# Optimization experiments

Measured on AMD Instinct MI355X. Metric: run time of the kernel, lower is better.

Reference implementation:

```python
import jax, jax.numpy as jnp
import numpy as np

DIM = 2048
N_HEADS = 16
Q_LORA = 1536
KV_LORA = 512
NOPE = 128
ROPE = 64
QK_HD = NOPE + ROPE  # 192
V_HD = 128
BS, SEQ = 2, 2048
EPS = 1e-6


def rmsnorm(x, w):
    var = jnp.mean(jnp.square(x), axis=-1, keepdims=True)
    return x * jax.lax.rsqrt(var + EPS) * w


def rope_cos_sin(seq_len, dim, dtype):
    inv_freq = 1.0 / (10000.0 ** (jnp.arange(0, dim, 2, dtype=jnp.float32) / dim))
    t = jnp.arange(seq_len, dtype=jnp.float32)
    freqs = jnp.outer(t, inv_freq)            # [S, dim/2]
    emb = jnp.concatenate([freqs, freqs], -1)  # [S, dim]
    return jnp.cos(emb).astype(dtype), jnp.sin(emb).astype(dtype)


def rotate_half(x):
    x1, x2 = jnp.split(x, 2, axis=-1)
    return jnp.concatenate([-x2, x1], axis=-1)


def apply_rope(x, cos, sin):
    # x: [B, S, H, D]; cos/sin: [S, D] -> broadcast over B, H
    return x * cos[None, :, None, :] + rotate_half(x) * sin[None, :, None, :]


def setup_inputs() -> dict:
    key = jax.random.key(0)
    ks = jax.random.split(key, 8)
    s = 0.02
    return {
        "x": jax.random.normal(ks[0], (BS, SEQ, DIM), jnp.float32),
        "wq_a_w": jax.random.normal(ks[1], (Q_LORA, DIM), jnp.float32) * s,
        "wq_a_b": jnp.zeros((Q_LORA,), jnp.float32),
        "q_norm_w": jnp.ones((Q_LORA,), jnp.float32),
        "wq_b_w": jax.random.normal(ks[2], (N_HEADS * QK_HD, Q_LORA), jnp.float32) * s,
        "wq_b_b": jnp.zeros((N_HEADS * QK_HD,), jnp.float32),
        "wkv_a_w": jax.random.normal(ks[3], (KV_LORA + ROPE, DIM), jnp.float32) * s,
        "wkv_a_b": jnp.zeros((KV_LORA + ROPE,), jnp.float32),
        "kv_norm_w": jnp.ones((KV_LORA,), jnp.float32),
        "wkv_b_w": jax.random.normal(ks[4], (N_HEADS * (NOPE + V_HD), KV_LORA), jnp.float32) * s,
        "wkv_b_b": jnp.zeros((N_HEADS * (NOPE + V_HD),), jnp.float32),
        "wo_w": jax.random.normal(ks[5], (DIM, N_HEADS * V_HD), jnp.float32) * s,
        "wo_b": jnp.zeros((DIM,), jnp.float32),
    }


def reference(x, wq_a_w, wq_a_b, q_norm_w, wq_b_w, wq_b_b,
              wkv_a_w, wkv_a_b, kv_norm_w, wkv_b_w, wkv_b_b, wo_w, wo_b):
    bs, seq_len, _ = x.shape
    # Q path: low-rank down, RMSNorm, up
    q = x @ wq_a_w.T + wq_a_b
    q = rmsnorm(q, q_norm_w)
    q = q @ wq_b_w.T + wq_b_b
    q = q.reshape(bs, seq_len, N_HEADS, QK_HD)
    q_nope, q_pe = q[..., :NOPE], q[..., NOPE:]
    # KV path: joint low-rank + decoupled rope key
    kv = x @ wkv_a_w.T + wkv_a_b
    kv_c, k_pe = kv[..., :KV_LORA], kv[..., KV_LORA:]
    k_pe = k_pe[:, :, None, :]  # [B, S, 1, ROPE]
    cos, sin = rope_cos_sin(seq_len, ROPE, x.dtype)
    q_pe = apply_rope(q_pe, cos, sin)
    k_pe = apply_rope(k_pe, cos, sin)
    # naive mode: materialize per-head K/V
    kv_c = rmsnorm(kv_c, kv_norm_w)
    kvb = (kv_c @ wkv_b_w.T + wkv_b_b).reshape(bs, seq_len, N_HEADS, NOPE + V_HD)
    k_nope, v = kvb[..., :NOPE], kvb[..., NOPE:]
    q_full = jnp.concatenate([q_nope, q_pe], axis=-1)            # [B,S,H,192]
    k_full = jnp.concatenate(
        [k_nope, jnp.broadcast_to(k_pe, (bs, seq_len, N_HEADS, ROPE))], axis=-1)
    scale = 1.0 / np.sqrt(QK_HD)
    scores = jnp.einsum('bqhd,bkhd->bhqk', q_full, k_full) * scale
    causal = jnp.tril(jnp.ones((seq_len, seq_len), bool))
    scores = jnp.where(causal[None, None], scores, jnp.finfo(scores.dtype).min)
    attn = jax.nn.softmax(scores, axis=-1)
    out = jnp.einsum('bhqk,bkhd->bqhd', attn, v)
    out = out.reshape(bs, seq_len, N_HEADS * V_HD)
    return out @ wo_w.T + wo_b
```

## Files before the change

kernel.cpp:

```cpp
#include <hip/hip_runtime.h>

#define SEQ 2048
#define NHEADS 16

typedef __bf16 bf16;
typedef __bf16 bf16x8 __attribute__((ext_vector_type(8)));
typedef __bf16 bf16x4v __attribute__((ext_vector_type(4)));
typedef float f32x4 __attribute__((ext_vector_type(4)));
typedef unsigned short u16x4 __attribute__((ext_vector_type(4)));

static __device__ __forceinline__ float bf2f(unsigned short u) {
    union { unsigned u32; float f; } v; v.u32 = ((unsigned)u) << 16; return v.f;
}
static __device__ __forceinline__ unsigned short f2bf(float f) {
    union { float f; unsigned u; } v; v.f = f;
    unsigned u = v.u;
    unsigned r = u + 0x7fffu + ((u >> 16) & 1u);
    return (unsigned short)(r >> 16);
}

static __device__ __forceinline__ void g2l16(const unsigned short* g, unsigned short* l) {
    __builtin_amdgcn_global_load_lds(
        (const __attribute__((address_space(1))) unsigned int*)(unsigned long long)g,
        (__attribute__((address_space(3))) unsigned int*)(unsigned int)(unsigned long long)l,
        16, 0, 0);
}

__global__ void detect_dtype(const unsigned* __restrict__ qnw, int* __restrict__ flag) {
    if (threadIdx.x == 0 && blockIdx.x == 0)
        *flag = (qnw[0] == 0x3F800000u) ? 1 : 0;
}

struct CvtArgs {
    const void* src[13];
    unsigned short* dst[13];
    int n[13];
    int startblk[14];
};
__global__ __launch_bounds__(256) void to_bf16_all(CvtArgs a, const int* __restrict__ flag) {
    int bx = blockIdx.x;
    int t = 0;
    while (bx >= a.startblk[t + 1]) ++t;
    int base = (bx - a.startblk[t]) * 4096;
    int n = a.n[t];
    int hi = base + 4096; if (hi > n) hi = n;
    int cnt = hi - base;
    if (*flag) {
        const f32x4* s = (const f32x4*)a.src[t] + (base >> 2);
        u16x4* d = (u16x4*)(a.dst[t] + base);
        int c4 = cnt >> 2;
        for (int e = threadIdx.x; e < c4; e += 256) {
            f32x4 v = s[e];
            u16x4 o;
#pragma unroll
            for (int j = 0; j < 4; ++j) o[j] = f2bf(v[j]);
            d[e] = o;
        }
    } else {
        const uint4* s = (const uint4*)a.src[t] + (base >> 3);
        uint4* d = (uint4*)(a.dst[t] + base);
        int c8 = cnt >> 3;
        for (int e = threadIdx.x; e < c8; e += 256) d[e] = s[e];
    }
}

struct GemmP {
    const unsigned short* A; int lda;
    const unsigned short* W;
    const unsigned short* bias;
    unsigned short* C; float* Cf; int ldc;
    int N; int K; const int* flagp;
    int nbx;
};

static __device__ void gemm_body(const GemmP g, int bx, int by,
                                 unsigned short* Al, unsigned short* Bl)
{
    const int lane = threadIdx.x & 63;
    const int w    = threadIdx.x >> 6;
    const int r    = lane & 15;
    const int quad = lane >> 4;
    const int m0 = by << 7;
    const int n0 = bx << 7;
    const int wr = (w >> 1) << 6;
    const int wc = (w & 1) << 6;

    const int srow = lane >> 2;
    const int scol = (lane & 3) << 3;
    const int j0 = w * 2, j1 = w * 2 + 1;

    const unsigned short* a0 = g.A + (size_t)(m0 + j0 * 16 + srow) * g.lda + scol;
    const unsigned short* a1 = g.A + (size_t)(m0 + j1 * 16 + srow) * g.lda + scol;
    int bn0 = n0 + j0 * 16 + srow; if (bn0 >= g.N) bn0 = g.N - 1;
    int bn1 = n0 + j1 * 16 + srow; if (bn1 >= g.N) bn1 = g.N - 1;
    const unsigned short* b0 = g.W + (size_t)bn0 * g.K + scol;
    const unsigned short* b1 = g.W + (size_t)bn1 * g.K + scol;

    f32x4 acc[4][4];
#pragma unroll
    for (int mt = 0; mt < 4; ++mt)
#pragma unroll
        for (int nt = 0; nt < 4; ++nt) acc[mt][nt] = (f32x4){0.f, 0.f, 0.f, 0.f};

    for (int kb = 0; kb < g.K; kb += 32) {
        __syncthreads();
        g2l16(a0 + kb, &Al[j0 * 512 + lane * 8]);
        g2l16(a1 + kb, &Al[j1 * 512 + lane * 8]);
        g2l16(b0 + kb, &Bl[j0 * 512 + lane * 8]);
        g2l16(b1 + kb, &Bl[j1 * 512 + lane * 8]);
        __syncthreads();

        bf16x8 af[4], bfr[4];
#pragma unroll
        for (int mt = 0; mt < 4; ++mt)
            af[mt] = *(const bf16x8*)&Al[(wr + mt * 16 + r) * 32 + quad * 8];
#pragma unroll
        for (int nt = 0; nt < 4; ++nt)
            bfr[nt] = *(const bf16x8*)&Bl[(wc + nt * 16 + r) * 32 + quad * 8];
#pragma unroll
        for (int mt = 0; mt < 4; ++mt)
#pragma unroll
            for (int nt = 0; nt < 4; ++nt)
                acc[mt][nt] = __builtin_amdgcn_mfma_f32_16x16x32_bf16(af[mt], bfr[nt], acc[mt][nt], 0, 0, 0);
    }

    int outf = (g.Cf && g.flagp) ? *g.flagp : 0;
    float bv[4];
#pragma unroll
    for (int nt = 0; nt < 4; ++nt) {
        int col = n0 + wc + nt * 16 + r;
        bv[nt] = (g.bias && col < g.N) ? bf2f(g.bias[col]) : 0.f;
    }
#pragma unroll
    for (int mt = 0; mt < 4; ++mt) {
#pragma unroll
        for (int i = 0; i < 4; ++i) {
            int row = m0 + wr + mt * 16 + quad * 4 + i;
#pragma unroll
            for (int nt = 0; nt < 4; ++nt) {
                int col = n0 + wc + nt * 16 + r;
                if (col < g.N) {
                    float v = acc[mt][nt][i] + bv[nt];
                    size_t idx = (size_t)row * g.ldc + col;
                    if (g.Cf) {
                        if (outf) g.Cf[idx] = v;
                        else      ((unsigned short*)g.Cf)[idx] = f2bf(v);
                    } else {
                        g.C[idx] = f2bf(v);
                    }
                }
            }
        }
    }
}

__global__ __launch_bounds__(256) void gemm_one(GemmP g) {
    __shared__ unsigned short Al[128 * 32];
    __shared__ unsigned short Bl[128 * 32];
    gemm_body(g, blockIdx.x, blockIdx.y, Al, Bl);
}

__global__ __launch_bounds__(256) void gemm_two(GemmP g0, GemmP g1, int nblk0) {
    __shared__ unsigned short Al[128 * 32];
    __shared__ unsigned short Bl[128 * 32];
    int id = blockIdx.x;
    if (id < nblk0) {
        gemm_body(g0, id % g0.nbx, id / g0.nbx, Al, Bl);
    } else {
        id -= nblk0;
        gemm_body(g1, id % g1.nbx, id / g1.nbx, Al, Bl);
    }
}

__global__ __launch_bounds__(256) void rmsnorm_ip2(
    unsigned short* __restrict__ d0, int s0w, int w0w, const unsigned short* __restrict__ w0,
    unsigned short* __restrict__ d1, int s1w, int w1w, const unsigned short* __restrict__ w1,
    int rows0)
{
    __shared__ float red[256];
    int row = blockIdx.x;
    unsigned short* p; const unsigned short* wt; int stride, width;
    if (row < rows0) { p = d0; wt = w0; stride = s0w; width = w0w; }
    else { row -= rows0; p = d1; wt = w1; stride = s1w; width = w1w; }
    p += (size_t)row * stride;

    float ss = 0.f;
    for (int j = threadIdx.x; j < width; j += 256) {
        float f = bf2f(p[j]);
        ss += f * f;
    }
    red[threadIdx.x] = ss;
    __syncthreads();
    for (int s = 128; s > 0; s >>= 1) {
        if ((int)threadIdx.x < s) red[threadIdx.x] += red[threadIdx.x + s];
        __syncthreads();
    }
    float rstd = rsqrtf(red[0] / (float)width + 1e-6f);
    for (int j = threadIdx.x; j < width; j += 256) {
        p[j] = f2bf(bf2f(p[j]) * rstd * bf2f(wt[j]));
    }
}

__global__ __launch_bounds__(256) void rope_ip_all(
    unsigned short* __restrict__ qbuf, unsigned short* __restrict__ kvbf)
{
    int row = blockIdx.x;
    int s = row & (SEQ - 1);
    for (int t = threadIdx.x; t < 544; t += 256) {
        int i = t & 31;
        float inv = exp2f(-(float)i * (13.2877123795f / 32.0f));
        float ang = (float)s * inv;
        float c = cosf(ang), sn = sinf(ang);
        unsigned short* p;
        if (t < 512) p = qbuf + (size_t)row * 3072 + (t >> 5) * 192 + 128;
        else         p = kvbf + (size_t)row * 576 + 512;
        float x1 = bf2f(p[i]), x2 = bf2f(p[i + 32]);
        p[i]      = f2bf(x1 * c - x2 * sn);
        p[i + 32] = f2bf(x2 * c + x1 * sn);
    }
}

__global__ __launch_bounds__(256) void mla_attn_mfma(
    const unsigned short* __restrict__ qbuf,
    const unsigned short* __restrict__ kvb,
    const unsigned short* __restrict__ kvbuf,
    unsigned short* __restrict__ attn_out)
{
    __shared__ unsigned short Kt[2][32 * 200];
    __shared__ unsigned short Vt[2][128 * 40];
    __shared__ unsigned short Pm[4][16 * 40];

    const int bh = blockIdx.y;
    const int b = bh >> 4, h = bh & 15;
    const int tid  = threadIdx.x;
    const int lane = tid & 63;
    const int w    = tid >> 6;
    const int r    = lane & 15;
    const int quad = lane >> 4;
    const int rowk0 = b * SEQ;
    const float scale = 0.0721687836487f;

    int kldso[3];
    const unsigned short* ksrc[3];
    int krst[3];
#pragma unroll
    for (int j = 0; j < 3; ++j) {
        int v = tid + j * 256;
        int row = v / 24, c = v % 24;
        kldso[j] = row * 200 + c * 8;
        if (c < 16) { ksrc[j] = kvb + (size_t)(rowk0 + row) * 4096 + h * 256 + c * 8; krst[j] = 4096; }
        else        { ksrc[j] = kvbuf + (size_t)(rowk0 + row) * 576 + 512 + (c - 16) * 8; krst[j] = 576; }
    }
    const int vp  = tid & 15;
    const int vdc = tid >> 4;
    const unsigned short* vsrc = kvb + (size_t)(rowk0 + 2 * vp) * 4096 + h * 256 + 128 + vdc * 8;

    unsigned short* Pw = Pm[w];

#pragma unroll 1
    for (int half = 0; half < 2; ++half) {
        const int qt = half ? (31 - (int)blockIdx.x) : (int)blockIdx.x;
        const int qbase = qt * 64 + w * 16;
        const int nkb = 2 * qt + 2;
        const int itmax = 2 * qt + (w >> 1);

        bf16x8 qf[6];
        {
            const unsigned short* qp =
                qbuf + (size_t)(rowk0 + qbase + r) * 3072 + h * 192 + quad * 8;
#pragma unroll
            for (int t = 0; t < 6; ++t) {
                bf16x8 v = *(const bf16x8*)(qp + t * 32);
#pragma unroll
                for (int j = 0; j < 8; ++j) v[j] = (__bf16)((float)v[j] * scale);
                qf[t] = v;
            }
        }

        f32x4 O[8];
#pragma unroll
        for (int f = 0; f < 8; ++f) O[f] = (f32x4){0.f, 0.f, 0.f, 0.f};
        float mi = -1e30f, li = 0.f;

        uint4 pk0, pk1, pk2, pv0, pv1;

        __syncthreads();
        pk0 = *(const uint4*)(ksrc[0]);
        pk1 = *(const uint4*)(ksrc[1]);
        pk2 = *(const uint4*)(ksrc[2]);
        pv0 = *(const uint4*)(vsrc);
        pv1 = *(const uint4*)(vsrc + 4096);
        {
            *(uint4*)&Kt[0][kldso[0]] = pk0;
            *(uint4*)&Kt[0][kldso[1]] = pk1;
            *(uint4*)&Kt[0][kldso[2]] = pk2;
            const unsigned* ea = (const unsigned*)&pv0;
            const unsigned* eb = (const unsigned*)&pv1;
#pragma unroll
            for (int t = 0; t < 4; ++t) {
                unsigned pe = (ea[t] & 0xffffu) | (eb[t] << 16);
                unsigned po = (ea[t] >> 16) | (eb[t] & 0xffff0000u);
                *(unsigned*)&Vt[0][(vdc * 8 + 2 * t) * 40 + 2 * vp]     = pe;
                *(unsigned*)&Vt[0][(vdc * 8 + 2 * t + 1) * 40 + 2 * vp] = po;
            }
        }
        __syncthreads();

#pragma unroll 1
        for (int it = 0; it < nkb; ++it) {
            const int p = it & 1;
            const int kb = it * 32;
            const bool more = (it + 1 < nkb);

            if (more) {
                const size_t koff = (size_t)(kb + 32);
                pk0 = *(const uint4*)(ksrc[0] + koff * krst[0]);
                pk1 = *(const uint4*)(ksrc[1] + koff * krst[1]);
                pk2 = *(const uint4*)(ksrc[2] + koff * krst[2]);
                pv0 = *(const uint4*)(vsrc + koff * 4096);
                pv1 = *(const uint4*)(vsrc + koff * 4096 + 4096);
            }

            if (it <= itmax) {
                f32x4 s0 = {0.f, 0.f, 0.f, 0.f}, s1 = {0.f, 0.f, 0.f, 0.f};
                __builtin_amdgcn_s_setprio(1);
#pragma unroll
                for (int t = 0; t < 6; ++t) {
                    bf16x8 k0 = *(const bf16x8*)&Kt[p][r * 200 + t * 32 + quad * 8];
                    bf16x8 k1 = *(const bf16x8*)&Kt[p][(16 + r) * 200 + t * 32 + quad * 8];
                    s0 = __builtin_amdgcn_mfma_f32_16x16x32_bf16(k0, qf[t], s0, 0, 0, 0);
                    s1 = __builtin_amdgcn_mfma_f32_16x16x32_bf16(k1, qf[t], s1, 0, 0, 0);
                }
                __builtin_amdgcn_s_setprio(0);

                const int qrow = qbase + r;
                float a0[4], a1[4];
                float mx = -1e30f;
                if (kb + 31 > qbase) {
#pragma unroll
                    for (int i = 0; i < 4; ++i) {
                        a0[i] = (kb + quad * 4 + i      <= qrow) ? s0[i] : -1e30f;
                        a1[i] = (kb + 16 + quad * 4 + i <= qrow) ? s1[i] : -1e30f;
                        mx = fmaxf(mx, fmaxf(a0[i], a1[i]));
                    }
                } else {
#pragma unroll
                    for (int i = 0; i < 4; ++i) {
                        a0[i] = s0[i];
                        a1[i] = s1[i];
                        mx = fmaxf(mx, fmaxf(a0[i], a1[i]));
                    }
                }
                mx = fmaxf(mx, __shfl_xor(mx, 16, 64));
                mx = fmaxf(mx, __shfl_xor(mx, 32, 64));

                if (!__all(mx <= mi + 8.f)) {
                    float mn = fmaxf(mi, mx);
                    float al = __expf(mi - mn);
#pragma unroll
                    for (int f = 0; f < 8; ++f) O[f] *= al;
                    li *= al;
                    mi = mn;
                }

                float p0[4], p1[4], ps = 0.f;
#pragma unroll
                for (int i = 0; i < 4; ++i) {
                    p0[i] = __expf(a0[i] - mi);
                    p1[i] = __expf(a1[i] - mi);
                    ps += p0[i] + p1[i];
                }
                ps += __shfl_xor(ps, 16, 64);
                ps += __shfl_xor(ps, 32, 64);
                li += ps;

                bf16x4v b0v, b1v;
#pragma unroll
                for (int i = 0; i < 4; ++i) {
                    b0v[i] = (__bf16)p0[i];
                    b1v[i] = (__bf16)p1[i];
                }
                *(bf16x4v*)&Pw[r * 40 + quad * 4]      = b0v;
                *(bf16x4v*)&Pw[r * 40 + 16 + quad * 4] = b1v;

                bf16x8 pf = *(const bf16x8*)&Pw[r * 40 + quad * 8];
                __builtin_amdgcn_s_setprio(1);
#pragma unroll
                for (int f = 0; f < 8; ++f) {
                    bf16x8 vb = *(const bf16x8*)&Vt[p][(f * 16 + r) * 40 + quad * 8];
                    O[f] = __builtin_amdgcn_mfma_f32_16x16x32_bf16(vb, pf, O[f], 0, 0, 0);
                }
                __builtin_amdgcn_s_setprio(0);
            }

            if (more) {
                const int q2 = 1 - p;
                *(uint4*)&Kt[q2][kldso[0]] = pk0;
                *(uint4*)&Kt[q2][kldso[1]] = pk1;
                *(uint4*)&Kt[q2][kldso[2]] = pk2;
                const unsigned* ea = (const unsigned*)&pv0;
                const unsigned* eb = (const unsigned*)&pv1;
#pragma unroll
                for (int t = 0; t < 4; ++t) {
                    unsigned pe = (ea[t] & 0xffffu) | (eb[t] << 16);
                    unsigned po = (ea[t] >> 16) | (eb[t] & 0xffff0000u);
                    *(unsigned*)&Vt[q2][(vdc * 8 + 2 * t) * 40 + 2 * vp]     = pe;
                    *(unsigned*)&Vt[q2][(vdc * 8 + 2 * t + 1) * 40 + 2 * vp] = po;
                }
                __syncthreads();
            }
        }

        float inv = (li > 0.f) ? (1.f / li) : 0.f;
        unsigned short* orow = attn_out + (size_t)(rowk0 + qbase + r) * 2048 + h * 128;
#pragma unroll
        for (int f = 0; f < 8; ++f) {
            bf16x4v o;
#pragma unroll
            for (int i = 0; i < 4; ++i) o[i] = (__bf16)(O[f][i] * inv);
            *(bf16x4v*)&orow[f * 16 + quad * 4] = o;
        }
    }
}

extern "C" void kernel_launch(void* const* d_in, const int* in_sizes, int n_in,
                              void* d_out, int out_size, void* d_ws, size_t ws_size,
                              hipStream_t stream)
{
    char* ws = (char*)d_ws;
    size_t off = 0;
    auto alloc = [&](size_t bytes) -> void* {
        void* p = ws + off;
        off = (off + bytes + 255) & ~(size_t)255;
        return p;
    };

    int* flag = (int*)alloc(256);

    const int nx = 4096 * 2048;
    unsigned short* xb    = (unsigned short*)alloc((size_t)nx * 2);
    unsigned short* wqa   = (unsigned short*)alloc((size_t)1536 * 2048 * 2);
    unsigned short* wqab  = (unsigned short*)alloc(1536 * 2);
    unsigned short* qnw   = (unsigned short*)alloc(1536 * 2);
    unsigned short* wqb   = (unsigned short*)alloc((size_t)3072 * 1536 * 2);
    unsigned short* wqbb  = (unsigned short*)alloc(3072 * 2);
    unsigned short* wkva  = (unsigned short*)alloc((size_t)576 * 2048 * 2);
    unsigned short* wkvab = (unsigned short*)alloc(576 * 2);
    unsigned short* kvnw  = (unsigned short*)alloc(512 * 2);
    unsigned short* wkvb  = (unsigned short*)alloc((size_t)4096 * 512 * 2);
    unsigned short* wkvbb = (unsigned short*)alloc(4096 * 2);
    unsigned short* wo    = (unsigned short*)alloc((size_t)2048 * 2048 * 2);
    unsigned short* wob   = (unsigned short*)alloc(2048 * 2);

    unsigned short* qa   = (unsigned short*)alloc((size_t)4096 * 1536 * 2);
    unsigned short* qbuf = (unsigned short*)alloc((size_t)4096 * 3072 * 2);
    unsigned short* kvbf = (unsigned short*)alloc((size_t)4096 * 576 * 2);
    unsigned short* kvb  = (unsigned short*)alloc((size_t)4096 * 4096 * 2);
    unsigned short* attn = xb;

    const int M = 4096;
    dim3 blk(256);

    detect_dtype<<<dim3(1), dim3(64), 0, stream>>>((const unsigned*)d_in[3], flag);

    {
        CvtArgs a;
        unsigned short* dsts[13] = {xb, wqa, wqab, qnw, wqb, wqbb, wkva, wkvab, kvnw, wkvb, wkvbb, wo, wob};
        int pb = 0;
        for (int i = 0; i < 13; ++i) {
            a.src[i] = d_in[i];
            a.dst[i] = dsts[i];
            a.n[i] = in_sizes[i];
            a.startblk[i] = pb;
            pb += (in_sizes[i] + 4095) / 4096;
        }
        a.startblk[13] = pb;
        to_bf16_all<<<dim3(pb), blk, 0, stream>>>(a, flag);
    }

    auto mkg = [](const unsigned short* A, int lda, const unsigned short* W,
                  const unsigned short* bias, unsigned short* C, float* Cf, int ldc,
                  int N, int K, const int* fl) -> GemmP {
        GemmP g;
        g.A = A; g.lda = lda; g.W = W; g.bias = bias;
        g.C = C; g.Cf = Cf; g.ldc = ldc; g.N = N; g.K = K; g.flagp = fl;
        g.nbx = (N + 127) / 128;
        return g;
    };

    {
        GemmP gqa  = mkg(xb, 2048, wqa,  wqab,  qa,   nullptr, 1536, 1536, 2048, nullptr);
        GemmP gkva = mkg(xb, 2048, wkva, wkvab, kvbf, nullptr, 576,  576,  2048, nullptr);
        int nb0 = gqa.nbx * (M / 128), nb1 = gkva.nbx * (M / 128);
        gemm_two<<<dim3(nb0 + nb1), blk, 0, stream>>>(gqa, gkva, nb0);
    }

    rmsnorm_ip2<<<dim3(2 * M), blk, 0, stream>>>(qa, 1536, 1536, qnw,
                                                 kvbf, 576, 512, kvnw, M);

    {
        GemmP gqb  = mkg(qa,   1536, wqb,  wqbb,  qbuf, nullptr, 3072, 3072, 1536, nullptr);
        GemmP gkvb = mkg(kvbf, 576,  wkvb, wkvbb, kvb,  nullptr, 4096, 4096, 512,  nullptr);
        int nb0 = gqb.nbx * (M / 128), nb1 = gkvb.nbx * (M / 128);
        gemm_two<<<dim3(nb0 + nb1), blk, 0, stream>>>(gqb, gkvb, nb0);
    }

    rope_ip_all<<<dim3(M), blk, 0, stream>>>(qbuf, kvbf);

    mla_attn_mfma<<<dim3(16, 2 * NHEADS), blk, 0, stream>>>(qbuf, kvb, kvbf, attn);

    {
        GemmP gout = mkg(attn, 2048, wo, wob, nullptr, (float*)d_out, 2048, 2048, 2048, flag);
        gemm_one<<<dim3(gout.nbx, M / 128), blk, 0, stream>>>(gout);
    }
}
```

Before: 492.4 us.

## Double-buffer GEMM LDS loads, vectorize RMSNorm, and repack attention LDS layouts

```diff
diff --git a/kernel.cpp b/kernel.cpp
--- a/kernel.cpp
+++ b/kernel.cpp
@@ -8,6 +8,7 @@
 typedef __bf16 bf16x4v __attribute__((ext_vector_type(4)));
 typedef float f32x4 __attribute__((ext_vector_type(4)));
 typedef unsigned short u16x4 __attribute__((ext_vector_type(4)));
+typedef unsigned short u16x8 __attribute__((ext_vector_type(8)));
 
 static __device__ __forceinline__ float bf2f(unsigned short u) {
     union { unsigned u32; float f; } v; v.u32 = ((unsigned)u) << 16; return v.f;
@@ -102,26 +103,38 @@
 #pragma unroll
         for (int nt = 0; nt < 4; ++nt) acc[mt][nt] = (f32x4){0.f, 0.f, 0.f, 0.f};
 
+    auto stage = [&](int buf, int kb) {
+        unsigned short* Ad = Al + (buf << 12);
+        unsigned short* Bd = Bl + (buf << 12);
+        g2l16(a0 + kb, &Ad[j0 * 512 + lane * 8]);
+        g2l16(a1 + kb, &Ad[j1 * 512 + lane * 8]);
+        g2l16(b0 + kb, &Bd[j0 * 512 + lane * 8]);
+        g2l16(b1 + kb, &Bd[j1 * 512 + lane * 8]);
+    };
+
+    stage(0, 0);
+    __syncthreads();
+    int cur = 0;
     for (int kb = 0; kb < g.K; kb += 32) {
-        __syncthreads();
-        g2l16(a0 + kb, &Al[j0 * 512 + lane * 8]);
-        g2l16(a1 + kb, &Al[j1 * 512 + lane * 8]);
-        g2l16(b0 + kb, &Bl[j0 * 512 + lane * 8]);
-        g2l16(b1 + kb, &Bl[j1 * 512 + lane * 8]);
-        __syncthreads();
-
+        if (kb + 32 < g.K) stage(cur ^ 1, kb + 32);
+
+        const unsigned short* As = Al + (cur << 12);
+        const unsigned short* Bs = Bl + (cur << 12);
         bf16x8 af[4], bfr[4];
 #pragma unroll
         for (int mt = 0; mt < 4; ++mt)
-            af[mt] = *(const bf16x8*)&Al[(wr + mt * 16 + r) * 32 + quad * 8];
+            af[mt] = *(const bf16x8*)&As[(wr + mt * 16 + r) * 32 + quad * 8];
 #pragma unroll
         for (int nt = 0; nt < 4; ++nt)
-            bfr[nt] = *(const bf16x8*)&Bl[(wc + nt * 16 + r) * 32 + quad * 8];
+            bfr[nt] = *(const bf16x8*)&Bs[(wc + nt * 16 + r) * 32 + quad * 8];
 #pragma unroll
         for (int mt = 0; mt < 4; ++mt)
 #pragma unroll
             for (int nt = 0; nt < 4; ++nt)
                 acc[mt][nt] = __builtin_amdgcn_mfma_f32_16x16x32_bf16(af[mt], bfr[nt], acc[mt][nt], 0, 0, 0);
+
+        __syncthreads();
+        cur ^= 1;
     }
 
     int outf = (g.Cf && g.flagp) ? *g.flagp : 0;
@@ -155,14 +168,14 @@
 }
 
 __global__ __launch_bounds__(256) void gemm_one(GemmP g) {
-    __shared__ unsigned short Al[128 * 32];
-    __shared__ unsigned short Bl[128 * 32];
+    __shared__ unsigned short Al[2 * 4096];
+    __shared__ unsigned short Bl[2 * 4096];
     gemm_body(g, blockIdx.x, blockIdx.y, Al, Bl);
 }
 
 __global__ __launch_bounds__(256) void gemm_two(GemmP g0, GemmP g1, int nblk0) {
-    __shared__ unsigned short Al[128 * 32];
-    __shared__ unsigned short Bl[128 * 32];
+    __shared__ unsigned short Al[2 * 4096];
+    __shared__ unsigned short Bl[2 * 4096];
     int id = blockIdx.x;
     if (id < nblk0) {
         gemm_body(g0, id % g0.nbx, id / g0.nbx, Al, Bl);
@@ -184,10 +197,15 @@
     else { row -= rows0; p = d1; wt = w1; stride = s1w; width = w1w; }
     p += (size_t)row * stride;
 
+    const int nv = width >> 3;
+    u16x8* pv = (u16x8*)p;
+    const u16x8* wv = (const u16x8*)wt;
+
     float ss = 0.f;
-    for (int j = threadIdx.x; j < width; j += 256) {
-        float f = bf2f(p[j]);
-        ss += f * f;
+    for (int j = threadIdx.x; j < nv; j += 256) {
+        u16x8 v = pv[j];
+#pragma unroll
+        for (int k = 0; k < 8; ++k) { float f = bf2f(v[k]); ss += f * f; }
     }
     red[threadIdx.x] = ss;
     __syncthreads();
@@ -196,8 +214,11 @@
         __syncthreads();
     }
     float rstd = rsqrtf(red[0] / (float)width + 1e-6f);
-    for (int j = threadIdx.x; j < width; j += 256) {
-        p[j] = f2bf(bf2f(p[j]) * rstd * bf2f(wt[j]));
+    for (int j = threadIdx.x; j < nv; j += 256) {
+        u16x8 v = pv[j], g = wv[j], o;
+#pragma unroll
+        for (int k = 0; k < 8; ++k) o[k] = f2bf(bf2f(v[k]) * rstd * bf2f(g[k]));
+        pv[j] = o;
     }
 }
 
@@ -226,9 +247,9 @@
     const unsigned short* __restrict__ kvbuf,
     unsigned short* __restrict__ attn_out)
 {
-    __shared__ unsigned short Kt[2][32 * 200];
-    __shared__ unsigned short Vt[2][128 * 40];
-    __shared__ unsigned short Pm[4][16 * 40];
+    __shared__ unsigned short Kt[2][6144];
+    __shared__ unsigned short Vt[2][4096];
+    __shared__ unsigned short Pm[4][512];
 
     const int bh = blockIdx.y;
     const int b = bh >> 4, h = bh & 15;
@@ -245,17 +266,40 @@
     int krst[3];
 #pragma unroll
     for (int j = 0; j < 3; ++j) {
-        int v = tid + j * 256;
-        int row = v / 24, c = v % 24;
-        kldso[j] = row * 200 + c * 8;
+        int idx = tid + j * 256;
+        int clo = idx & 3, rlo = (idx >> 2) & 1, rest = idx >> 3;
+        int c   = (rest % 6) * 4 + clo;
+        int row = (rest / 6) * 2 + rlo;
+        kldso[j] = (c >> 2) * 1024 + row * 32 + (c & 3) * 8;
         if (c < 16) { ksrc[j] = kvb + (size_t)(rowk0 + row) * 4096 + h * 256 + c * 8; krst[j] = 4096; }
         else        { ksrc[j] = kvbuf + (size_t)(rowk0 + row) * 576 + 512 + (c - 16) * 8; krst[j] = 576; }
     }
     const int vp  = tid & 15;
     const int vdc = tid >> 4;
     const unsigned short* vsrc = kvb + (size_t)(rowk0 + 2 * vp) * 4096 + h * 256 + 128 + vdc * 8;
+    const int vwbase = (vdc >> 1) * 512 + (8 * (vdc & 1)) * 32
+                     + ((2 * vp) ^ (16 * (vdc & 1)));
+
+    auto stageK = [&](int buf, const uint4& k0, const uint4& k1, const uint4& k2) {
+        *(uint4*)&Kt[buf][kldso[0]] = k0;
+        *(uint4*)&Kt[buf][kldso[1]] = k1;
+        *(uint4*)&Kt[buf][kldso[2]] = k2;
+    };
+    auto stageV = [&](int buf, const uint4& va, const uint4& vb_) {
+        const unsigned* ea = (const unsigned*)&va;
+        const unsigned* eb = (const unsigned*)&vb_;
+        unsigned short* Vd = &Vt[buf][0];
+#pragma unroll
+        for (int t = 0; t < 4; ++t) {
+            unsigned pe = (ea[t] & 0xffffu) | (eb[t] << 16);
+            unsigned po = (ea[t] >> 16) | (eb[t] & 0xffff0000u);
+            *(unsigned*)&Vd[vwbase + (2 * t) * 32]     = pe;
+            *(unsigned*)&Vd[vwbase + (2 * t + 1) * 32] = po;
+        }
+    };
 
     unsigned short* Pw = Pm[w];
+    const int vqx = (quad ^ (2 * ((r >> 3) & 1))) * 8;
 
 #pragma unroll 1
     for (int half = 0; half < 2; ++half) {
@@ -290,20 +334,8 @@
         pk2 = *(const uint4*)(ksrc[2]);
         pv0 = *(const uint4*)(vsrc);
         pv1 = *(const uint4*)(vsrc + 4096);
-        {
-            *(uint4*)&Kt[0][kldso[0]] = pk0;
-            *(uint4*)&Kt[0][kldso[1]] = pk1;
-            *(uint4*)&Kt[0][kldso[2]] = pk2;
-            const unsigned* ea = (const unsigned*)&pv0;
-            const unsigned* eb = (const unsigned*)&pv1;
-#pragma unroll
-            for (int t = 0; t < 4; ++t) {
-                unsigned pe = (ea[t] & 0xffffu) | (eb[t] << 16);
-                unsigned po = (ea[t] >> 16) | (eb[t] & 0xffff0000u);
-                *(unsigned*)&Vt[0][(vdc * 8 + 2 * t) * 40 + 2 * vp]     = pe;
-                *(unsigned*)&Vt[0][(vdc * 8 + 2 * t + 1) * 40 + 2 * vp] = po;
-            }
-        }
+        stageK(0, pk0, pk1, pk2);
+        stageV(0, pv0, pv1);
         __syncthreads();
 
 #pragma unroll 1
@@ -326,8 +358,8 @@
                 __builtin_amdgcn_s_setprio(1);
 #pragma unroll
                 for (int t = 0; t < 6; ++t) {
-                    bf16x8 k0 = *(const bf16x8*)&Kt[p][r * 200 + t * 32 + quad * 8];
-                    bf16x8 k1 = *(const bf16x8*)&Kt[p][(16 + r) * 200 + t * 32 + quad * 8];
+                    bf16x8 k0 = *(const bf16x8*)&Kt[p][t * 1024 + r * 32 + quad * 8];
+                    bf16x8 k1 = *(const bf16x8*)&Kt[p][t * 1024 + 512 + r * 32 + quad * 8];
                     s0 = __builtin_amdgcn_mfma_f32_16x16x32_bf16(k0, qf[t], s0, 0, 0, 0);
                     s1 = __builtin_amdgcn_mfma_f32_16x16x32_bf16(k1, qf[t], s1, 0, 0, 0);
                 }
@@ -380,14 +412,14 @@
                     b0v[i] = (__bf16)p0[i];
                     b1v[i] = (__bf16)p1[i];
                 }
-                *(bf16x4v*)&Pw[r * 40 + quad * 4]      = b0v;
-                *(bf16x4v*)&Pw[r * 40 + 16 + quad * 4] = b1v;
-
-                bf16x8 pf = *(const bf16x8*)&Pw[r * 40 + quad * 8];
+                *(bf16x4v*)&Pw[r * 32 + quad * 4]      = b0v;
+                *(bf16x4v*)&Pw[r * 32 + 16 + quad * 4] = b1v;
+
+                bf16x8 pf = *(const bf16x8*)&Pw[r * 32 + quad * 8];
                 __builtin_amdgcn_s_setprio(1);
 #pragma unroll
                 for (int f = 0; f < 8; ++f) {
-                    bf16x8 vb = *(const bf16x8*)&Vt[p][(f * 16 + r) * 40 + quad * 8];
+                    bf16x8 vb = *(const bf16x8*)&Vt[p][f * 512 + r * 32 + vqx];
                     O[f] = __builtin_amdgcn_mfma_f32_16x16x32_bf16(vb, pf, O[f], 0, 0, 0);
                 }
                 __builtin_amdgcn_s_setprio(0);
@@ -395,18 +427,8 @@
 
             if (more) {
                 const int q2 = 1 - p;
-                *(uint4*)&Kt[q2][kldso[0]] = pk0;
-                *(uint4*)&Kt[q2][kldso[1]] = pk1;
-                *(uint4*)&Kt[q2][kldso[2]] = pk2;
-                const unsigned* ea = (const unsigned*)&pv0;
-                const unsigned* eb = (const unsigned*)&pv1;
-#pragma unroll
-                for (int t = 0; t < 4; ++t) {
-                    unsigned pe = (ea[t] & 0xffffu) | (eb[t] << 16);
-                    unsigned po = (ea[t] >> 16) | (eb[t] & 0xffff0000u);
-                    *(unsigned*)&Vt[q2][(vdc * 8 + 2 * t) * 40 + 2 * vp]     = pe;
-                    *(unsigned*)&Vt[q2][(vdc * 8 + 2 * t + 1) * 40 + 2 * vp] = po;
-                }
+                stageK(q2, pk0, pk1, pk2);
+                stageV(q2, pv0, pv1);
                 __syncthreads();
             }
         }
```

Measured after the change: 449.0 us. -8.8%, faster.
